# Optimization experiments

Hardware: AMD Instinct MI355X
Metric: run time of the kernel (lower is better)

## Reference

```python
import jax, jax.numpy as jnp
import numpy as np

# Static hypernetwork layer sizes from HyperOption(z_dim=256, inner_h=64, a_dim=32, layers=3)
SIZES = [256 * 64, 64, 64 * 64, 64, 64 * 32, 32]  # sum = 22688
SPLITS = np.cumsum(SIZES)[:-1]


def setup_inputs() -> dict:
    key = jax.random.key(0)
    ks = jax.random.split(key, 8)
    B, Z, H = 4096, 256, 1024
    return {
        "inputs": jax.random.normal(ks[0], (B, Z), dtype=jnp.float32),
        "option": jax.random.normal(ks[1], (B, sum(SIZES)), dtype=jnp.float32) * 0.05,
        "w1": jax.random.normal(ks[2], (H, Z), dtype=jnp.float32) * 0.05,
        "b1": jax.random.normal(ks[3], (H,), dtype=jnp.float32) * 0.05,
        "w2": jax.random.normal(ks[4], (H, H), dtype=jnp.float32) * 0.05,
        "b2": jax.random.normal(ks[5], (H,), dtype=jnp.float32) * 0.05,
        "w3": jax.random.normal(ks[6], (1, H), dtype=jnp.float32) * 0.05,
        "b3": jax.random.normal(ks[7], (1,), dtype=jnp.float32) * 0.05,
    }


def _apply_option(state, option):
    # Per-sample hypernetwork MLP: weights/biases packed in `option`.
    parts = jnp.split(option, SPLITS, axis=-1)
    cur = state
    n_layers = len(parts) // 2
    for i in range(n_layers):
        w = parts[2 * i].reshape(option.shape[0], -1, cur.shape[-1])  # [B, out, in]
        b = parts[2 * i + 1]                                          # [B, out]
        cur = jnp.einsum('boi,bi->bo', w, cur) + b
        if i < n_layers - 1:
            cur = jax.nn.relu(cur)
    return cur


def _value(z, w1, b1, w2, b2, w3, b3):
    t = jax.nn.elu(z @ w1.T + b1)
    t = jax.nn.elu(t @ w2.T + b2)
    return t @ w3.T + b3  # [B, 1]


def reference(inputs, option, w1, b1, w2, b2, w3, b3):
    value = _value(inputs, w1, b1, w2, b2, w3, b3)   # [B, 1]
    action = _apply_option(inputs, option)            # [B, 32]
    return jnp.concatenate([value, action], axis=-1)  # [B, 33]
```

## Files before the change

### kernel.cpp

```cpp
#include <hip/hip_runtime.h>
#include <hip/hip_bf16.h>
#include <cstdint>

typedef __attribute__((ext_vector_type(8))) short  short8;
typedef __attribute__((ext_vector_type(8))) __bf16 bf16x8;
typedef __attribute__((ext_vector_type(4))) float  floatx4;
typedef __attribute__((ext_vector_type(4))) float  f32x4;
typedef __attribute__((ext_vector_type(4))) short  short4v;

union Frag { short8 s; bf16x8 b; };

__device__ inline short f2bf(float f) {
    union { float f; unsigned u; } v; v.f = f;
    unsigned r = (v.u + 0x7fffu + ((v.u >> 16) & 1u)) >> 16;
    return (short)r;
}
__device__ inline float elu(float x) { return x > 0.f ? x : __expf(x) - 1.f; }

__device__ inline short8 load8_f32_to_bf16(const float* __restrict__ p) {
    float4 f0 = ((const float4*)p)[0];
    float4 f1 = ((const float4*)p)[1];
    short8 r;
    r[0] = f2bf(f0.x); r[1] = f2bf(f0.y); r[2] = f2bf(f0.z); r[3] = f2bf(f0.w);
    r[4] = f2bf(f1.x); r[5] = f2bf(f1.y); r[6] = f2bf(f1.z); r[7] = f2bf(f1.w);
    return r;
}
__device__ inline float dot4(f32x4 a, f32x4 b) {
    return a.x * b.x + a.y * b.y + a.z * b.z + a.w * b.w;
}
__device__ inline f32x4 ntload4(const f32x4* __restrict__ p) {
    return __builtin_nontemporal_load(p);
}
__device__ inline float ntload1(const float* __restrict__ p) {
    return __builtin_nontemporal_load(p);
}

#define B_SZ   4096
#define Z_DIM  256
#define H_DIM  1024
#define OUT_W  33
#define OFF_W1 0
#define OFF_B1 16384
#define OFF_W2 16448
#define OFF_B2 20544
#define OFF_W3 20608
#define OFF_B3 22656
#define OPT_W  22688

#define HYP_K1 1024
#define G_BLOCKS 256
#define CONV_BLOCKS 64

__device__ __forceinline__ int xcd_remap(int i) {
    return (i & 7) * 32 + (i >> 3);
}

template<int KTOT, bool ACONV, bool BCONV, bool VEPI>
__device__ __forceinline__ void gemm_tile(
    const void* __restrict__ Av, const void* __restrict__ Bv,
    const float* __restrict__ bias, const float* __restrict__ w3,
    __hip_bfloat16* __restrict__ T, float* __restrict__ out,
    int bm, int bn, int tid)
{
    const int lane = tid & 63, wid = tid >> 6;
    const int wm = wid >> 1, wn = wid & 1;
    const int m_wave = bm * 128 + wm * 64;
    const int n_wave = bn * 128 + wn * 64;
    const int lr = lane & 15, lk = (lane >> 4) * 8;

    floatx4 acc[4][4] = {};
    for (int k0 = 0; k0 < KTOT; k0 += 32) {
        Frag a[4], bb[4];
#pragma unroll
        for (int sm = 0; sm < 4; ++sm) {
            const size_t off = (size_t)(m_wave + sm * 16 + lr) * KTOT + k0 + lk;
            if constexpr (ACONV) a[sm].s = load8_f32_to_bf16((const float*)Av + off);
            else                 a[sm].s = *(const short8*)((const ushort*)Av + off);
        }
#pragma unroll
        for (int sn = 0; sn < 4; ++sn) {
            const size_t off = (size_t)(n_wave + sn * 16 + lr) * KTOT + k0 + lk;
            if constexpr (BCONV) bb[sn].s = load8_f32_to_bf16((const float*)Bv + off);
            else                 bb[sn].s = *(const short8*)((const ushort*)Bv + off);
        }
#pragma unroll
        for (int sm = 0; sm < 4; ++sm)
#pragma unroll
            for (int sn = 0; sn < 4; ++sn)
                acc[sm][sn] = __builtin_amdgcn_mfma_f32_16x16x32_bf16(
                    a[sm].b, bb[sn].b, acc[sm][sn], 0, 0, 0);
    }

    if constexpr (VEPI) {
        float bias_v[4], w3_v[4];
#pragma unroll
        for (int sn = 0; sn < 4; ++sn) {
            const int n = n_wave + sn * 16 + lr;
            bias_v[sn] = bias[n];
            w3_v[sn]   = w3[n];
        }
#pragma unroll
        for (int sm = 0; sm < 4; ++sm) {
#pragma unroll
            for (int r = 0; r < 4; ++r) {
                float rowsum = 0.f;
#pragma unroll
                for (int sn = 0; sn < 4; ++sn)
                    rowsum += elu(acc[sm][sn][r] + bias_v[sn]) * w3_v[sn];
                rowsum += __shfl_xor(rowsum, 1);
                rowsum += __shfl_xor(rowsum, 2);
                rowsum += __shfl_xor(rowsum, 4);
                rowsum += __shfl_xor(rowsum, 8);
                if (lr == 0) {
                    const int m = m_wave + sm * 16 + (lane >> 4) * 4 + r;
                    atomicAdd(out + (size_t)m * OUT_W, rowsum);
                }
            }
        }
    } else {
#pragma unroll
        for (int sm = 0; sm < 4; ++sm)
#pragma unroll
            for (int sn = 0; sn < 4; ++sn) {
                const int n = n_wave + sn * 16 + lr;
                const float bv = bias[n];
#pragma unroll
                for (int r = 0; r < 4; ++r) {
                    const int m = m_wave + sm * 16 + (lane >> 4) * 4 + r;
                    T[(size_t)m * H_DIM + n] = __float2bfloat16(elu(acc[sm][sn][r] + bv));
                }
            }
    }
}

__device__ __forceinline__ void hyper_sample(
    const float* __restrict__ z, const float* __restrict__ opt,
    float* __restrict__ out, int b, int tid,
    float* __restrict__ h1, float* __restrict__ h2)
{
    const int lane = tid & 63, w = tid >> 6;
    const int l16 = lane & 15, lg = lane >> 4;
    const float* __restrict__ orow = opt + (size_t)b * OPT_W;

    const f32x4* __restrict__ Z4 = (const f32x4*)(z + (size_t)b * Z_DIM);
    f32x4 zv[4];
#pragma unroll
    for (int p = 0; p < 4; ++p) zv[p] = Z4[p * 16 + l16];

    {
        const f32x4* __restrict__ W = (const f32x4*)(orow + OFF_W1) + (size_t)(w * 16) * 64;
        f32x4 wv[16];
#pragma unroll
        for (int g = 0; g < 4; ++g)
#pragma unroll
            for (int p = 0; p < 4; ++p)
                wv[g * 4 + p] = ntload4(W + (g * 4 + lg) * 64 + p * 16 + l16);
#pragma unroll
        for (int g = 0; g < 4; ++g) {
            float acc = 0.f;
#pragma unroll
            for (int p = 0; p < 4; ++p) acc += dot4(wv[g * 4 + p], zv[p]);
            acc += __shfl_xor(acc, 1);
            acc += __shfl_xor(acc, 2);
            acc += __shfl_xor(acc, 4);
            acc += __shfl_xor(acc, 8);
            const int r = 16 * w + g * 4 + lg;
            if (l16 == 0) h1[r] = fmaxf(acc + ntload1(orow + OFF_B1 + r), 0.f);
        }
    }
    __syncthreads();

    {
        const f32x4 h1v = *(const f32x4*)(h1 + 4 * l16);
        const f32x4* __restrict__ W = (const f32x4*)(orow + OFF_W2 + w * 16 * 64);
        f32x4 wv[4];
#pragma unroll
        for (int j = 0; j < 4; ++j) wv[j] = ntload4(W + j * 64 + lane);
#pragma unroll
        for (int j = 0; j < 4; ++j) {
            float p = dot4(wv[j], h1v);
            p += __shfl_xor(p, 1); p += __shfl_xor(p, 2);
            p += __shfl_xor(p, 4); p += __shfl_xor(p, 8);
            const int r = 16 * w + j * 4 + lg;
            if (l16 == 0) h2[r] = fmaxf(p + ntload1(orow + OFF_B2 + r), 0.f);
        }
    }
    __syncthreads();

    {
        const f32x4 h2v = *(const f32x4*)(h2 + 4 * l16);
        const f32x4* __restrict__ W = (const f32x4*)(orow + OFF_W3 + w * 8 * 64);
        f32x4 wv[2];
#pragma unroll
        for (int j = 0; j < 2; ++j) wv[j] = ntload4(W + j * 64 + lane);
#pragma unroll
        for (int j = 0; j < 2; ++j) {
            float p = dot4(wv[j], h2v);
            p += __shfl_xor(p, 1); p += __shfl_xor(p, 2);
            p += __shfl_xor(p, 4); p += __shfl_xor(p, 8);
            const int r = 8 * w + j * 4 + lg;
            if (l16 == 0) out[(size_t)b * OUT_W + 1 + r] = p + ntload1(orow + OFF_B3 + r);
        }
    }
}

__global__ __launch_bounds__(256) void k1_kernel(
    const float* __restrict__ z, const float* __restrict__ opt,
    const float* __restrict__ w1, const float* __restrict__ b1,
    const float* __restrict__ w2, const float* __restrict__ b3,
    __hip_bfloat16* __restrict__ T1, __hip_bfloat16* __restrict__ w2bf,
    float* __restrict__ out)
{
    __shared__ float h1[64], h2[64];
    const int blk = blockIdx.x, t = threadIdx.x;

    if (blk < G_BLOCKS) {
        const int j = xcd_remap(blk);
        gemm_tile<Z_DIM, true, true, false>(z, w1, b1, nullptr, T1, nullptr,
                                            j >> 3, j & 7, t);
    } else if (blk < G_BLOCKS + CONV_BLOCKS) {
        const int gtid = (blk - G_BLOCKS) * 256 + t;
        if (gtid < B_SZ) out[(size_t)gtid * OUT_W] = b3[0];
#pragma unroll
        for (int i = 0; i < 16; ++i) {
            const int v = gtid + i * 16384;
            float4 f = ((const float4*)w2)[v];
            short4v s;
            s[0] = f2bf(f.x); s[1] = f2bf(f.y); s[2] = f2bf(f.z); s[3] = f2bf(f.w);
            ((short4v*)w2bf)[v] = s;
        }
    } else {
        hyper_sample(z, opt, out, blk - (G_BLOCKS + CONV_BLOCKS), t, h1, h2);
    }
}

__global__ __launch_bounds__(256) void k2_kernel(
    const float* __restrict__ z, const float* __restrict__ opt,
    const __hip_bfloat16* __restrict__ T1, const __hip_bfloat16* __restrict__ w2bf,
    const float* __restrict__ b2, const float* __restrict__ w3,
    float* __restrict__ out)
{
    __shared__ float h1[64], h2[64];
    const int blk = blockIdx.x, t = threadIdx.x;

    if (blk < G_BLOCKS) {
        const int j = xcd_remap(blk);
        gemm_tile<H_DIM, false, false, true>(T1, w2bf, b2, w3, nullptr, out,
                                             j >> 3, j & 7, t);
    } else {
        hyper_sample(z, opt, out, HYP_K1 + (blk - G_BLOCKS), t, h1, h2);
    }
}

extern "C" void kernel_launch(void* const* d_in, const int* in_sizes, int n_in,
                              void* d_out, int out_size, void* d_ws, size_t ws_size,
                              hipStream_t stream)
{
    const float* z   = (const float*)d_in[0];
    const float* opt = (const float*)d_in[1];
    const float* w1  = (const float*)d_in[2];
    const float* b1  = (const float*)d_in[3];
    const float* w2  = (const float*)d_in[4];
    const float* b2  = (const float*)d_in[5];
    const float* w3  = (const float*)d_in[6];
    const float* b3  = (const float*)d_in[7];
    float* out = (float*)d_out;

    __hip_bfloat16* T1   = (__hip_bfloat16*)d_ws;
    __hip_bfloat16* w2bf = (__hip_bfloat16*)((char*)d_ws +
                             (size_t)B_SZ * H_DIM * sizeof(__hip_bfloat16));

    k1_kernel<<<dim3(G_BLOCKS + CONV_BLOCKS + HYP_K1), dim3(256), 0, stream>>>(
        z, opt, w1, b1, w2, b3, T1, w2bf, out);

    k2_kernel<<<dim3(G_BLOCKS + (B_SZ - HYP_K1)), dim3(256), 0, stream>>>(
        z, opt, T1, w2bf, b2, w3, out);
}
```

Measured before the change: 117.4 us.

## Split hypernetwork into its own kernel and shrink second GEMM tiles to 128x64

Replaces the two mixed kernels, which interleaved GEMM tiles with hypernetwork per-sample blocks, with three launches. The first does GEMM1 plus the W2 conversion, the second does all 4096 hypernetwork samples, and the third does GEMM2. GEMM2 now uses 128x64 tiles across 512 blocks with a new XCD remap, which raises block count and occupancy for the K=1024 GEMM. The cost is an extra launch and the loss of overlap between the bandwidth-bound hypernetwork work and the compute-bound GEMM work.

```diff
diff --git a/kernel.cpp b/kernel.cpp
--- a/kernel.cpp
+++ b/kernel.cpp
@@ -47,15 +47,11 @@
 #define OFF_B3 22656
 #define OPT_W  22688
 
-#define HYP_K1 1024
-#define G_BLOCKS 256
+#define G1_BLOCKS 256
 #define CONV_BLOCKS 64
-
-__device__ __forceinline__ int xcd_remap(int i) {
-    return (i & 7) * 32 + (i >> 3);
-}
-
-template<int KTOT, bool ACONV, bool BCONV, bool VEPI>
+#define G2_BLOCKS 512
+
+template<int KTOT, int SM, int SN, bool ACONV, bool BCONV, bool VEPI>
 __device__ __forceinline__ void gemm_tile(
     const void* __restrict__ Av, const void* __restrict__ Bv,
     const float* __restrict__ bias, const float* __restrict__ w3,
@@ -64,48 +60,48 @@
 {
     const int lane = tid & 63, wid = tid >> 6;
     const int wm = wid >> 1, wn = wid & 1;
-    const int m_wave = bm * 128 + wm * 64;
-    const int n_wave = bn * 128 + wn * 64;
+    const int m_wave = bm * (32 * SM) + wm * (16 * SM);
+    const int n_wave = bn * (32 * SN) + wn * (16 * SN);
     const int lr = lane & 15, lk = (lane >> 4) * 8;
 
-    floatx4 acc[4][4] = {};
+    floatx4 acc[SM][SN] = {};
     for (int k0 = 0; k0 < KTOT; k0 += 32) {
-        Frag a[4], bb[4];
-#pragma unroll
-        for (int sm = 0; sm < 4; ++sm) {
+        Frag a[SM], bb[SN];
+#pragma unroll
+        for (int sm = 0; sm < SM; ++sm) {
             const size_t off = (size_t)(m_wave + sm * 16 + lr) * KTOT + k0 + lk;
             if constexpr (ACONV) a[sm].s = load8_f32_to_bf16((const float*)Av + off);
             else                 a[sm].s = *(const short8*)((const ushort*)Av + off);
         }
 #pragma unroll
-        for (int sn = 0; sn < 4; ++sn) {
+        for (int sn = 0; sn < SN; ++sn) {
             const size_t off = (size_t)(n_wave + sn * 16 + lr) * KTOT + k0 + lk;
             if constexpr (BCONV) bb[sn].s = load8_f32_to_bf16((const float*)Bv + off);
             else                 bb[sn].s = *(const short8*)((const ushort*)Bv + off);
         }
 #pragma unroll
-        for (int sm = 0; sm < 4; ++sm)
-#pragma unroll
-            for (int sn = 0; sn < 4; ++sn)
+        for (int sm = 0; sm < SM; ++sm)
+#pragma unroll
+            for (int sn = 0; sn < SN; ++sn)
                 acc[sm][sn] = __builtin_amdgcn_mfma_f32_16x16x32_bf16(
                     a[sm].b, bb[sn].b, acc[sm][sn], 0, 0, 0);
     }
 
     if constexpr (VEPI) {
-        float bias_v[4], w3_v[4];
-#pragma unroll
-        for (int sn = 0; sn < 4; ++sn) {
+        float bias_v[SN], w3_v[SN];
+#pragma unroll
+        for (int sn = 0; sn < SN; ++sn) {
             const int n = n_wave + sn * 16 + lr;
             bias_v[sn] = bias[n];
             w3_v[sn]   = w3[n];
         }
 #pragma unroll
-        for (int sm = 0; sm < 4; ++sm) {
+        for (int sm = 0; sm < SM; ++sm) {
 #pragma unroll
             for (int r = 0; r < 4; ++r) {
                 float rowsum = 0.f;
 #pragma unroll
-                for (int sn = 0; sn < 4; ++sn)
+                for (int sn = 0; sn < SN; ++sn)
                     rowsum += elu(acc[sm][sn][r] + bias_v[sn]) * w3_v[sn];
                 rowsum += __shfl_xor(rowsum, 1);
                 rowsum += __shfl_xor(rowsum, 2);
@@ -119,9 +115,9 @@
         }
     } else {
 #pragma unroll
-        for (int sm = 0; sm < 4; ++sm)
-#pragma unroll
-            for (int sn = 0; sn < 4; ++sn) {
+        for (int sm = 0; sm < SM; ++sm)
+#pragma unroll
+            for (int sn = 0; sn < SN; ++sn) {
                 const int n = n_wave + sn * 16 + lr;
                 const float bv = bias[n];
 #pragma unroll
@@ -204,22 +200,20 @@
     }
 }
 
-__global__ __launch_bounds__(256) void k1_kernel(
-    const float* __restrict__ z, const float* __restrict__ opt,
-    const float* __restrict__ w1, const float* __restrict__ b1,
-    const float* __restrict__ w2, const float* __restrict__ b3,
+__global__ __launch_bounds__(256) void kA_kernel(
+    const float* __restrict__ z, const float* __restrict__ w1,
+    const float* __restrict__ b1, const float* __restrict__ w2,
+    const float* __restrict__ b3,
     __hip_bfloat16* __restrict__ T1, __hip_bfloat16* __restrict__ w2bf,
     float* __restrict__ out)
 {
-    __shared__ float h1[64], h2[64];
     const int blk = blockIdx.x, t = threadIdx.x;
-
-    if (blk < G_BLOCKS) {
-        const int j = xcd_remap(blk);
-        gemm_tile<Z_DIM, true, true, false>(z, w1, b1, nullptr, T1, nullptr,
-                                            j >> 3, j & 7, t);
-    } else if (blk < G_BLOCKS + CONV_BLOCKS) {
-        const int gtid = (blk - G_BLOCKS) * 256 + t;
+    if (blk < G1_BLOCKS) {
+        const int j = (blk & 7) * 32 + (blk >> 3);
+        gemm_tile<Z_DIM, 4, 4, true, true, false>(z, w1, b1, nullptr, T1, nullptr,
+                                                  j >> 3, j & 7, t);
+    } else {
+        const int gtid = (blk - G1_BLOCKS) * 256 + t;
         if (gtid < B_SZ) out[(size_t)gtid * OUT_W] = b3[0];
 #pragma unroll
         for (int i = 0; i < 16; ++i) {
@@ -229,27 +223,26 @@
             s[0] = f2bf(f.x); s[1] = f2bf(f.y); s[2] = f2bf(f.z); s[3] = f2bf(f.w);
             ((short4v*)w2bf)[v] = s;
         }
-    } else {
-        hyper_sample(z, opt, out, blk - (G_BLOCKS + CONV_BLOCKS), t, h1, h2);
-    }
-}
-
-__global__ __launch_bounds__(256) void k2_kernel(
+    }
+}
+
+__global__ __launch_bounds__(256) void kB_kernel(
     const float* __restrict__ z, const float* __restrict__ opt,
+    float* __restrict__ out)
+{
+    __shared__ float h1[64], h2[64];
+    hyper_sample(z, opt, out, blockIdx.x, threadIdx.x, h1, h2);
+}
+
+__global__ __launch_bounds__(256) void kC_kernel(
     const __hip_bfloat16* __restrict__ T1, const __hip_bfloat16* __restrict__ w2bf,
     const float* __restrict__ b2, const float* __restrict__ w3,
     float* __restrict__ out)
 {
-    __shared__ float h1[64], h2[64];
     const int blk = blockIdx.x, t = threadIdx.x;
-
-    if (blk < G_BLOCKS) {
-        const int j = xcd_remap(blk);
-        gemm_tile<H_DIM, false, false, true>(T1, w2bf, b2, w3, nullptr, out,
-                                             j >> 3, j & 7, t);
-    } else {
-        hyper_sample(z, opt, out, HYP_K1 + (blk - G_BLOCKS), t, h1, h2);
-    }
+    const int j = (blk & 7) * 64 + (blk >> 3);
+    gemm_tile<H_DIM, 4, 2, false, false, true>(T1, w2bf, b2, w3, nullptr, out,
+                                               j >> 4, j & 15, t);
 }
 
 extern "C" void kernel_launch(void* const* d_in, const int* in_sizes, int n_in,
@@ -270,9 +263,10 @@
     __hip_bfloat16* w2bf = (__hip_bfloat16*)((char*)d_ws +
                              (size_t)B_SZ * H_DIM * sizeof(__hip_bfloat16));
 
-    k1_kernel<<<dim3(G_BLOCKS + CONV_BLOCKS + HYP_K1), dim3(256), 0, stream>>>(
-        z, opt, w1, b1, w2, b3, T1, w2bf, out);
-
-    k2_kernel<<<dim3(G_BLOCKS + (B_SZ - HYP_K1)), dim3(256), 0, stream>>>(
-        z, opt, T1, w2bf, b2, w3, out);
-}
+    kA_kernel<<<dim3(G1_BLOCKS + CONV_BLOCKS), dim3(256), 0, stream>>>(
+        z, w1, b1, w2, b3, T1, w2bf, out);
+
+    kB_kernel<<<dim3(B_SZ), dim3(256), 0, stream>>>(z, opt, out);
+
+    kC_kernel<<<dim3(G2_BLOCKS), dim3(256), 0, stream>>>(T1, w2bf, b2, w3, out);
+}
```

Result: slower. 135.5 us (+15.4%).
